# Kernel tuning notes

Measured on AMD Instinct MI355X. Metric: run time of the kernel, lower is better.

The kernel has to match this reference:

```python
import jax, jax.numpy as jnp
import numpy as np

N = 100000   # nodes
E = 1600000  # directed edges (avg degree 16)
IN, HID, OUT = 32, 64, 32


def setup_inputs() -> dict:
    key = jax.random.key(0)
    k0, k1, k2, k3 = jax.random.split(key, 4)
    x = jax.random.normal(k0, (N, IN), dtype=jnp.float32)
    edge_index = jax.random.randint(k1, (2, E), 0, N, dtype=jnp.int32)
    W1 = jax.random.normal(k2, (IN, HID), dtype=jnp.float32) * (1.0 / np.sqrt(IN))
    b1 = jnp.zeros((HID,), dtype=jnp.float32)
    W2 = jax.random.normal(k3, (HID, OUT), dtype=jnp.float32) * (1.0 / np.sqrt(HID))
    b2 = jnp.zeros((OUT,), dtype=jnp.float32)
    return {"x": x, "edge_index": edge_index, "W1": W1, "b1": b1, "W2": W2, "b2": b2}


def gcn_conv(x, src, dst, W, b, n):
    # GCNConv: D^{-1/2} (A + I) D^{-1/2} X W + b, deg computed after self-loops
    h = x @ W                                   # [N, d_out]
    ones = jnp.ones_like(dst, dtype=h.dtype)
    deg = jax.ops.segment_sum(ones, dst, num_segments=n)   # >= 1 (self-loops)
    dinv = jax.lax.rsqrt(jnp.maximum(deg, 1.0))
    norm = dinv[src] * dinv[dst]                # [E + N]
    agg = jax.ops.segment_sum(norm[:, None] * h[src], dst, num_segments=n)
    return agg + b


def reference(x, edge_index, W1, b1, W2, b2):
    n = x.shape[0]
    loop = jnp.arange(n, dtype=edge_index.dtype)
    src = jnp.concatenate([edge_index[0], loop])  # add self-loops once
    dst = jnp.concatenate([edge_index[1], loop])
    h = jax.nn.relu(gcn_conv(x, src, dst, W1, b1, n))
    # dropout omitted (eval mode)
    out = gcn_conv(h, src, dst, W2, b2, n)
    return out
```

## Files before the change

kernel.cpp:

```cpp
#include <hip/hip_runtime.h>

#define IN_F  32
#define HID_F 64
#define OUT_F 32

#define BKT_SHIFT 8
#define BKT_NODES 256
#define NBLK      128

__device__ inline unsigned short f2bf(float f) {
    unsigned u = __float_as_uint(f);
    return (unsigned short)((u + 0x7FFF + ((u >> 16) & 1)) >> 16);
}
__device__ inline float bf2f(unsigned short h) {
    return __uint_as_float(((unsigned)h) << 16);
}

__global__ __launch_bounds__(256) void count_kernel(const int* __restrict__ dst,
                                                    int* __restrict__ cnt, int E, int nb)
{
    __shared__ int hist[1024];
    int tid = threadIdx.x;
    for (int i = tid; i < nb; i += 256) hist[i] = 0;
    __syncthreads();
    for (int e = blockIdx.x * 256 + tid; e < E; e += NBLK * 256)
        atomicAdd(&hist[dst[e] >> BKT_SHIFT], 1);
    __syncthreads();
    for (int i = tid; i < nb; i += 256) cnt[i * NBLK + blockIdx.x] = hist[i];
}

__global__ __launch_bounds__(NBLK) void bsum_kernel(const int* __restrict__ cnt,
                                                    int* __restrict__ bsum)
{
    __shared__ int s[NBLK];
    int tid = threadIdx.x, b = blockIdx.x;
    s[tid] = cnt[b * NBLK + tid];
    __syncthreads();
    for (int off = NBLK / 2; off > 0; off >>= 1) {
        if (tid < off) s[tid] += s[tid + off];
        __syncthreads();
    }
    if (tid == 0) bsum[b] = s[0];
}

__global__ __launch_bounds__(512) void bscan_kernel(int* __restrict__ bsum, int nb,
                                                    int* __restrict__ cellstart, int nc,
                                                    int* __restrict__ rowstart, int n, int E)
{
    __shared__ int s[512];
    int tid = threadIdx.x;
    int my = (tid < nb) ? bsum[tid] : 0;
    s[tid] = my;
    __syncthreads();
    for (int off = 1; off < 512; off <<= 1) {
        int t = (tid >= off) ? s[tid - off] : 0;
        __syncthreads();
        s[tid] += t;
        __syncthreads();
    }
    if (tid < nb) bsum[tid] = s[tid] - my;
    if (tid == 0) { cellstart[nc] = E; rowstart[n] = E; }
}

__global__ __launch_bounds__(NBLK) void cscan_kernel(const int* __restrict__ cnt,
                                                     const int* __restrict__ bsum,
                                                     int* __restrict__ cellstart)
{
    __shared__ int s[NBLK];
    int tid = threadIdx.x, b = blockIdx.x;
    int my = cnt[b * NBLK + tid];
    s[tid] = my;
    __syncthreads();
    for (int off = 1; off < NBLK; off <<= 1) {
        int t = (tid >= off) ? s[tid - off] : 0;
        __syncthreads();
        s[tid] += t;
        __syncthreads();
    }
    cellstart[b * NBLK + tid] = bsum[b] + s[tid] - my;
}

__global__ __launch_bounds__(256) void append_kernel(
    const int* __restrict__ src, const int* __restrict__ dst,
    const int* __restrict__ cellstart, unsigned* __restrict__ pairs, int E, int nb)
{
    __shared__ int cur[1024];
    int tid = threadIdx.x;
    for (int i = tid; i < nb; i += 256) cur[i] = cellstart[i * NBLK + blockIdx.x];
    __syncthreads();
    for (int e = blockIdx.x * 256 + tid; e < E; e += NBLK * 256) {
        int d = dst[e];
        int pos = atomicAdd(&cur[d >> BKT_SHIFT], 1);
        pairs[pos] = ((unsigned)src[e] << BKT_SHIFT) | (unsigned)(d & (BKT_NODES - 1));
    }
}

__global__ __launch_bounds__(256) void place_kernel(
    const int* __restrict__ cellstart, const unsigned* __restrict__ pairs,
    int* __restrict__ srcs, int* __restrict__ rowstart, float* __restrict__ dinv, int n)
{
    __shared__ int hist[BKT_NODES];
    __shared__ int ofs[BKT_NODES];
    int b = blockIdx.x, tid = threadIdx.x;
    int beg = cellstart[b * NBLK], end = cellstart[(b + 1) * NBLK];
    hist[tid] = 0;
    __syncthreads();
    for (int e = beg + tid; e < end; e += 256)
        atomicAdd(&hist[pairs[e] & (BKT_NODES - 1)], 1);
    __syncthreads();
    int my = hist[tid];
    ofs[tid] = my;
    __syncthreads();
    for (int off = 1; off < 256; off <<= 1) {
        int t = (tid >= off) ? ofs[tid - off] : 0;
        __syncthreads();
        ofs[tid] += t;
        __syncthreads();
    }
    int excl = ofs[tid] - my;
    int node = b * BKT_NODES + tid;
    if (node < n) {
        rowstart[node] = beg + excl;
        dinv[node] = rsqrtf((float)(my + 1));
    }
    __syncthreads();
    ofs[tid] = excl;
    __syncthreads();
    for (int e = beg + tid; e < end; e += 256) {
        unsigned p = pairs[e];
        int dl = p & (BKT_NODES - 1);
        int pos = beg + atomicAdd(&ofs[dl], 1);
        srcs[pos] = (int)(p >> BKT_SHIFT);
    }
}

__global__ void xs_kernel(const float* __restrict__ x, const float* __restrict__ dinv,
                          unsigned short* __restrict__ xsb, int n) {
    int t = blockIdx.x * blockDim.x + threadIdx.x;
    if (t < n * (IN_F / 4)) {
        float d = dinv[t >> 3];
        float4 v = ((const float4*)x)[t];
        ushort4 o;
        o.x = f2bf(v.x * d); o.y = f2bf(v.y * d);
        o.z = f2bf(v.z * d); o.w = f2bf(v.w * d);
        ((ushort4*)xsb)[t] = o;
    }
}

__global__ __launch_bounds__(256) void fused1_kernel(
    const int* __restrict__ rowstart, const int* __restrict__ srcs,
    const unsigned short* __restrict__ xsb, const float* __restrict__ dinv,
    const float* __restrict__ b1, const float* __restrict__ W1,
    const float* __restrict__ W2, unsigned short* __restrict__ hs2b, int n)
{
    __shared__ float W1s[IN_F * HID_F];
    __shared__ float W2s[HID_F * OUT_F];
    __shared__ float grow[8][IN_F];
    __shared__ float hrow[8][HID_F];
    int tid = threadIdx.x;
    for (int t = tid; t < IN_F * HID_F; t += 256) W1s[t] = W1[t];
    for (int t = tid; t < HID_F * OUT_F; t += 256) W2s[t] = W2[t];

    int sub = tid >> 5;
    unsigned j = tid & 31;
    int node = blockIdx.x * 8 + sub;
    bool active = node < n;
    int nodec = active ? node : 0;

    int beg = rowstart[nodec], end = active ? rowstart[nodec + 1] : beg;
    float a0 = active ? bf2f(xsb[((unsigned)nodec << 5) + j]) : 0.f;
    float a1 = 0.f, a2 = 0.f, a3 = 0.f, a4 = 0.f, a5 = 0.f, a6 = 0.f, a7 = 0.f;
    int e = beg;
    for (; e + 8 <= end; e += 8) {
        unsigned o0 = ((unsigned)srcs[e]     << 5) + j, o1 = ((unsigned)srcs[e + 1] << 5) + j;
        unsigned o2 = ((unsigned)srcs[e + 2] << 5) + j, o3 = ((unsigned)srcs[e + 3] << 5) + j;
        unsigned o4 = ((unsigned)srcs[e + 4] << 5) + j, o5 = ((unsigned)srcs[e + 5] << 5) + j;
        unsigned o6 = ((unsigned)srcs[e + 6] << 5) + j, o7 = ((unsigned)srcs[e + 7] << 5) + j;
        a0 += bf2f(xsb[o0]); a1 += bf2f(xsb[o1]);
        a2 += bf2f(xsb[o2]); a3 += bf2f(xsb[o3]);
        a4 += bf2f(xsb[o4]); a5 += bf2f(xsb[o5]);
        a6 += bf2f(xsb[o6]); a7 += bf2f(xsb[o7]);
    }
    for (; e + 4 <= end; e += 4) {
        unsigned o0 = ((unsigned)srcs[e]     << 5) + j, o1 = ((unsigned)srcs[e + 1] << 5) + j;
        unsigned o2 = ((unsigned)srcs[e + 2] << 5) + j, o3 = ((unsigned)srcs[e + 3] << 5) + j;
        a0 += bf2f(xsb[o0]); a1 += bf2f(xsb[o1]);
        a2 += bf2f(xsb[o2]); a3 += bf2f(xsb[o3]);
    }
    for (; e < end; ++e) a0 += bf2f(xsb[((unsigned)srcs[e] << 5) + j]);
    float dv = dinv[nodec];
    grow[sub][j] = dv * (((a0 + a1) + (a2 + a3)) + ((a4 + a5) + (a6 + a7)));
    __syncthreads();

    float h0 = b1[j], h1v = b1[j + 32];
    #pragma unroll
    for (int k = 0; k < IN_F; ++k) {
        float gk = grow[sub][k];
        h0  += gk * W1s[k * HID_F + j];
        h1v += gk * W1s[k * HID_F + j + 32];
    }
    hrow[sub][j]      = fmaxf(h0, 0.f);
    hrow[sub][j + 32] = fmaxf(h1v, 0.f);
    __syncthreads();

    float p = 0.f;
    #pragma unroll
    for (int k = 0; k < HID_F; ++k) p += hrow[sub][k] * W2s[k * OUT_F + j];
    if (active) hs2b[((unsigned)node << 5) + j] = f2bf(dv * p);
}

__global__ __launch_bounds__(256) void agg2_kernel(
    const int* __restrict__ rowstart, const int* __restrict__ srcs,
    const unsigned short* __restrict__ hs2b, const float* __restrict__ dinv,
    const float* __restrict__ b2, float* __restrict__ out, int n)
{
    int t = blockIdx.x * blockDim.x + threadIdx.x;
    int node = t >> 5;
    if (node >= n) return;
    unsigned j = t & 31;
    int beg = rowstart[node], end = rowstart[node + 1];
    float a0 = bf2f(hs2b[((unsigned)node << 5) + j]);
    float a1 = 0.f, a2 = 0.f, a3 = 0.f, a4 = 0.f, a5 = 0.f, a6 = 0.f, a7 = 0.f;
    int e = beg;
    for (; e + 8 <= end; e += 8) {
        unsigned o0 = ((unsigned)srcs[e]     << 5) + j, o1 = ((unsigned)srcs[e + 1] << 5) + j;
        unsigned o2 = ((unsigned)srcs[e + 2] << 5) + j, o3 = ((unsigned)srcs[e + 3] << 5) + j;
        unsigned o4 = ((unsigned)srcs[e + 4] << 5) + j, o5 = ((unsigned)srcs[e + 5] << 5) + j;
        unsigned o6 = ((unsigned)srcs[e + 6] << 5) + j, o7 = ((unsigned)srcs[e + 7] << 5) + j;
        a0 += bf2f(hs2b[o0]); a1 += bf2f(hs2b[o1]);
        a2 += bf2f(hs2b[o2]); a3 += bf2f(hs2b[o3]);
        a4 += bf2f(hs2b[o4]); a5 += bf2f(hs2b[o5]);
        a6 += bf2f(hs2b[o6]); a7 += bf2f(hs2b[o7]);
    }
    for (; e + 4 <= end; e += 4) {
        unsigned o0 = ((unsigned)srcs[e]     << 5) + j, o1 = ((unsigned)srcs[e + 1] << 5) + j;
        unsigned o2 = ((unsigned)srcs[e + 2] << 5) + j, o3 = ((unsigned)srcs[e + 3] << 5) + j;
        a0 += bf2f(hs2b[o0]); a1 += bf2f(hs2b[o1]);
        a2 += bf2f(hs2b[o2]); a3 += bf2f(hs2b[o3]);
    }
    for (; e < end; ++e) a0 += bf2f(hs2b[((unsigned)srcs[e] << 5) + j]);
    out[(size_t)node * OUT_F + j] =
        dinv[node] * (((a0 + a1) + (a2 + a3)) + ((a4 + a5) + (a6 + a7))) + b2[j];
}

extern "C" void kernel_launch(void* const* d_in, const int* in_sizes, int n_in,
                              void* d_out, int out_size, void* d_ws, size_t ws_size,
                              hipStream_t stream) {
    const float* x  = (const float*)d_in[0];
    const int*   ei = (const int*)  d_in[1];
    const float* W1 = (const float*)d_in[2];
    const float* b1 = (const float*)d_in[3];
    const float* W2 = (const float*)d_in[4];
    const float* b2 = (const float*)d_in[5];
    float* out = (float*)d_out;

    const int n = in_sizes[0] / IN_F;
    const int E = in_sizes[1] / 2;
    const int* src = ei;
    const int* dst = ei + E;

    const int nb = (n + BKT_NODES - 1) >> BKT_SHIFT;
    const int nc = nb * NBLK;

    int* ip = (int*)d_ws;
    int* cnt       = ip;                 ip += nc;
    int* cellstart = ip;                 ip += nc + 1;
    int* bsum      = ip;                 ip += nb + 1;
    int* rowstart  = ip;                 ip += n + 1;
    unsigned* pairs = (unsigned*)ip;     ip += E;
    int* srcs_srt  = ip;                 ip += E;
    float* dinv = (float*)ip;            ip += n;
    unsigned short* xsb  = (unsigned short*)ip;
    ip += (size_t)n * IN_F / 2;
    unsigned short* hs2b = (unsigned short*)ip;

    count_kernel<<<NBLK, 256, 0, stream>>>(dst, cnt, E, nb);
    bsum_kernel <<<nb, NBLK, 0, stream>>>(cnt, bsum);
    bscan_kernel<<<1, 512, 0, stream>>>(bsum, nb, cellstart, nc, rowstart, n, E);
    cscan_kernel<<<nb, NBLK, 0, stream>>>(cnt, bsum, cellstart);
    append_kernel<<<NBLK, 256, 0, stream>>>(src, dst, cellstart, pairs, E, nb);
    place_kernel<<<nb, 256, 0, stream>>>(cellstart, pairs, srcs_srt, rowstart, dinv, n);

    xs_kernel<<<((size_t)n * 8 + 255) / 256, 256, 0, stream>>>(x, dinv, xsb, n);

    fused1_kernel<<<(n + 7) / 8, 256, 0, stream>>>(rowstart, srcs_srt, xsb, dinv, b1, W1, W2, hs2b, n);
    agg2_kernel<<<((size_t)n * 32 + 255) / 256, 256, 0, stream>>>(rowstart, srcs_srt, hs2b, dinv, b2, out, n);
}
```

Before: 256.4 us.

## Gather two bf16 features per lane with 16 lanes per node in aggregations

Both aggregation kernels now assign 16 threads per node and load packed 32-bit words holding two bf16 features, instead of 32 threads loading single 16-bit values. fused1 processes 16 nodes per block and its dense stages are remapped accordingly, with packed bf16 writes. The intent is to halve the per-edge load instruction count and make each row gather a 64-byte access with wider transactions. The cost is more accumulator registers per thread and more FMA work per thread in the dense stages.

```diff
diff --git a/kernel.cpp b/kernel.cpp
--- a/kernel.cpp
+++ b/kernel.cpp
@@ -12,9 +12,8 @@
     unsigned u = __float_as_uint(f);
     return (unsigned short)((u + 0x7FFF + ((u >> 16) & 1)) >> 16);
 }
-__device__ inline float bf2f(unsigned short h) {
-    return __uint_as_float(((unsigned)h) << 16);
-}
+__device__ inline float bflo(unsigned w) { return __uint_as_float(w << 16); }
+__device__ inline float bfhi(unsigned w) { return __uint_as_float(w & 0xFFFF0000u); }
 
 __global__ __launch_bounds__(256) void count_kernel(const int* __restrict__ dst,
                                                     int* __restrict__ cnt, int E, int nb)
@@ -149,98 +148,131 @@
 
 __global__ __launch_bounds__(256) void fused1_kernel(
     const int* __restrict__ rowstart, const int* __restrict__ srcs,
-    const unsigned short* __restrict__ xsb, const float* __restrict__ dinv,
+    const unsigned* __restrict__ xs2, const float* __restrict__ dinv,
     const float* __restrict__ b1, const float* __restrict__ W1,
-    const float* __restrict__ W2, unsigned short* __restrict__ hs2b, int n)
+    const float* __restrict__ W2, unsigned* __restrict__ hs2p, int n)
 {
     __shared__ float W1s[IN_F * HID_F];
     __shared__ float W2s[HID_F * OUT_F];
-    __shared__ float grow[8][IN_F];
-    __shared__ float hrow[8][HID_F];
+    __shared__ float grow[16][IN_F];
+    __shared__ float hrow[16][HID_F];
     int tid = threadIdx.x;
     for (int t = tid; t < IN_F * HID_F; t += 256) W1s[t] = W1[t];
     for (int t = tid; t < HID_F * OUT_F; t += 256) W2s[t] = W2[t];
 
-    int sub = tid >> 5;
-    unsigned j = tid & 31;
-    int node = blockIdx.x * 8 + sub;
+    int nl = tid >> 4;
+    unsigned q = tid & 15;
+    int node = blockIdx.x * 16 + nl;
     bool active = node < n;
     int nodec = active ? node : 0;
 
     int beg = rowstart[nodec], end = active ? rowstart[nodec + 1] : beg;
-    float a0 = active ? bf2f(xsb[((unsigned)nodec << 5) + j]) : 0.f;
-    float a1 = 0.f, a2 = 0.f, a3 = 0.f, a4 = 0.f, a5 = 0.f, a6 = 0.f, a7 = 0.f;
+    unsigned ws = active ? xs2[((unsigned)nodec << 4) + q] : 0u;
+    float a0l = bflo(ws), a0h = bfhi(ws);
+    float a1l = 0.f, a1h = 0.f, a2l = 0.f, a2h = 0.f, a3l = 0.f, a3h = 0.f;
+    float a4l = 0.f, a4h = 0.f, a5l = 0.f, a5h = 0.f, a6l = 0.f, a6h = 0.f;
+    float a7l = 0.f, a7h = 0.f;
     int e = beg;
     for (; e + 8 <= end; e += 8) {
-        unsigned o0 = ((unsigned)srcs[e]     << 5) + j, o1 = ((unsigned)srcs[e + 1] << 5) + j;
-        unsigned o2 = ((unsigned)srcs[e + 2] << 5) + j, o3 = ((unsigned)srcs[e + 3] << 5) + j;
-        unsigned o4 = ((unsigned)srcs[e + 4] << 5) + j, o5 = ((unsigned)srcs[e + 5] << 5) + j;
-        unsigned o6 = ((unsigned)srcs[e + 6] << 5) + j, o7 = ((unsigned)srcs[e + 7] << 5) + j;
-        a0 += bf2f(xsb[o0]); a1 += bf2f(xsb[o1]);
-        a2 += bf2f(xsb[o2]); a3 += bf2f(xsb[o3]);
-        a4 += bf2f(xsb[o4]); a5 += bf2f(xsb[o5]);
-        a6 += bf2f(xsb[o6]); a7 += bf2f(xsb[o7]);
+        unsigned o0 = ((unsigned)srcs[e]     << 4) + q, o1 = ((unsigned)srcs[e + 1] << 4) + q;
+        unsigned o2 = ((unsigned)srcs[e + 2] << 4) + q, o3 = ((unsigned)srcs[e + 3] << 4) + q;
+        unsigned o4 = ((unsigned)srcs[e + 4] << 4) + q, o5 = ((unsigned)srcs[e + 5] << 4) + q;
+        unsigned o6 = ((unsigned)srcs[e + 6] << 4) + q, o7 = ((unsigned)srcs[e + 7] << 4) + q;
+        unsigned w0 = xs2[o0], w1 = xs2[o1], w2 = xs2[o2], w3 = xs2[o3];
+        unsigned w4 = xs2[o4], w5 = xs2[o5], w6 = xs2[o6], w7 = xs2[o7];
+        a0l += bflo(w0); a0h += bfhi(w0); a1l += bflo(w1); a1h += bfhi(w1);
+        a2l += bflo(w2); a2h += bfhi(w2); a3l += bflo(w3); a3h += bfhi(w3);
+        a4l += bflo(w4); a4h += bfhi(w4); a5l += bflo(w5); a5h += bfhi(w5);
+        a6l += bflo(w6); a6h += bfhi(w6); a7l += bflo(w7); a7h += bfhi(w7);
     }
     for (; e + 4 <= end; e += 4) {
-        unsigned o0 = ((unsigned)srcs[e]     << 5) + j, o1 = ((unsigned)srcs[e + 1] << 5) + j;
-        unsigned o2 = ((unsigned)srcs[e + 2] << 5) + j, o3 = ((unsigned)srcs[e + 3] << 5) + j;
-        a0 += bf2f(xsb[o0]); a1 += bf2f(xsb[o1]);
-        a2 += bf2f(xsb[o2]); a3 += bf2f(xsb[o3]);
-    }
-    for (; e < end; ++e) a0 += bf2f(xsb[((unsigned)srcs[e] << 5) + j]);
+        unsigned o0 = ((unsigned)srcs[e]     << 4) + q, o1 = ((unsigned)srcs[e + 1] << 4) + q;
+        unsigned o2 = ((unsigned)srcs[e + 2] << 4) + q, o3 = ((unsigned)srcs[e + 3] << 4) + q;
+        unsigned w0 = xs2[o0], w1 = xs2[o1], w2 = xs2[o2], w3 = xs2[o3];
+        a0l += bflo(w0); a0h += bfhi(w0); a1l += bflo(w1); a1h += bfhi(w1);
+        a2l += bflo(w2); a2h += bfhi(w2); a3l += bflo(w3); a3h += bfhi(w3);
+    }
+    for (; e < end; ++e) {
+        unsigned w0 = xs2[((unsigned)srcs[e] << 4) + q];
+        a0l += bflo(w0); a0h += bfhi(w0);
+    }
     float dv = dinv[nodec];
-    grow[sub][j] = dv * (((a0 + a1) + (a2 + a3)) + ((a4 + a5) + (a6 + a7)));
-    __syncthreads();
-
-    float h0 = b1[j], h1v = b1[j + 32];
+    grow[nl][2 * q]     = dv * (((a0l + a1l) + (a2l + a3l)) + ((a4l + a5l) + (a6l + a7l)));
+    grow[nl][2 * q + 1] = dv * (((a0h + a1h) + (a2h + a3h)) + ((a4h + a5h) + (a6h + a7h)));
+    __syncthreads();
+
+    float h0 = b1[q], h1 = b1[q + 16], h2 = b1[q + 32], h3 = b1[q + 48];
     #pragma unroll
     for (int k = 0; k < IN_F; ++k) {
-        float gk = grow[sub][k];
-        h0  += gk * W1s[k * HID_F + j];
-        h1v += gk * W1s[k * HID_F + j + 32];
-    }
-    hrow[sub][j]      = fmaxf(h0, 0.f);
-    hrow[sub][j + 32] = fmaxf(h1v, 0.f);
-    __syncthreads();
-
-    float p = 0.f;
+        float gk = grow[nl][k];
+        h0 += gk * W1s[k * HID_F + q];
+        h1 += gk * W1s[k * HID_F + q + 16];
+        h2 += gk * W1s[k * HID_F + q + 32];
+        h3 += gk * W1s[k * HID_F + q + 48];
+    }
+    hrow[nl][q]      = fmaxf(h0, 0.f);
+    hrow[nl][q + 16] = fmaxf(h1, 0.f);
+    hrow[nl][q + 32] = fmaxf(h2, 0.f);
+    hrow[nl][q + 48] = fmaxf(h3, 0.f);
+    __syncthreads();
+
+    float p0 = 0.f, p1 = 0.f;
     #pragma unroll
-    for (int k = 0; k < HID_F; ++k) p += hrow[sub][k] * W2s[k * OUT_F + j];
-    if (active) hs2b[((unsigned)node << 5) + j] = f2bf(dv * p);
+    for (int k = 0; k < HID_F; ++k) {
+        float hk = hrow[nl][k];
+        p0 += hk * W2s[k * OUT_F + 2 * q];
+        p1 += hk * W2s[k * OUT_F + 2 * q + 1];
+    }
+    if (active) {
+        unsigned pack = (unsigned)f2bf(dv * p0) | ((unsigned)f2bf(dv * p1) << 16);
+        hs2p[((unsigned)node << 4) + q] = pack;
+    }
 }
 
 __global__ __launch_bounds__(256) void agg2_kernel(
     const int* __restrict__ rowstart, const int* __restrict__ srcs,
-    const unsigned short* __restrict__ hs2b, const float* __restrict__ dinv,
+    const unsigned* __restrict__ hs2p, const float* __restrict__ dinv,
     const float* __restrict__ b2, float* __restrict__ out, int n)
 {
     int t = blockIdx.x * blockDim.x + threadIdx.x;
-    int node = t >> 5;
+    int node = t >> 4;
     if (node >= n) return;
-    unsigned j = t & 31;
+    unsigned q = t & 15;
     int beg = rowstart[node], end = rowstart[node + 1];
-    float a0 = bf2f(hs2b[((unsigned)node << 5) + j]);
-    float a1 = 0.f, a2 = 0.f, a3 = 0.f, a4 = 0.f, a5 = 0.f, a6 = 0.f, a7 = 0.f;
+    unsigned ws = hs2p[((unsigned)node << 4) + q];
+    float a0l = bflo(ws), a0h = bfhi(ws);
+    float a1l = 0.f, a1h = 0.f, a2l = 0.f, a2h = 0.f, a3l = 0.f, a3h = 0.f;
+    float a4l = 0.f, a4h = 0.f, a5l = 0.f, a5h = 0.f, a6l = 0.f, a6h = 0.f;
+    float a7l = 0.f, a7h = 0.f;
     int e = beg;
     for (; e + 8 <= end; e += 8) {
-        unsigned o0 = ((unsigned)srcs[e]     << 5) + j, o1 = ((unsigned)srcs[e + 1] << 5) + j;
-        unsigned o2 = ((unsigned)srcs[e + 2] << 5) + j, o3 = ((unsigned)srcs[e + 3] << 5) + j;
-        unsigned o4 = ((unsigned)srcs[e + 4] << 5) + j, o5 = ((unsigned)srcs[e + 5] << 5) + j;
-        unsigned o6 = ((unsigned)srcs[e + 6] << 5) + j, o7 = ((unsigned)srcs[e + 7] << 5) + j;
-        a0 += bf2f(hs2b[o0]); a1 += bf2f(hs2b[o1]);
-        a2 += bf2f(hs2b[o2]); a3 += bf2f(hs2b[o3]);
-        a4 += bf2f(hs2b[o4]); a5 += bf2f(hs2b[o5]);
-        a6 += bf2f(hs2b[o6]); a7 += bf2f(hs2b[o7]);
+        unsigned o0 = ((unsigned)srcs[e]     << 4) + q, o1 = ((unsigned)srcs[e + 1] << 4) + q;
+        unsigned o2 = ((unsigned)srcs[e + 2] << 4) + q, o3 = ((unsigned)srcs[e + 3] << 4) + q;
+        unsigned o4 = ((unsigned)srcs[e + 4] << 4) + q, o5 = ((unsigned)srcs[e + 5] << 4) + q;
+        unsigned o6 = ((unsigned)srcs[e + 6] << 4) + q, o7 = ((unsigned)srcs[e + 7] << 4) + q;
+        unsigned w0 = hs2p[o0], w1 = hs2p[o1], w2 = hs2p[o2], w3 = hs2p[o3];
+        unsigned w4 = hs2p[o4], w5 = hs2p[o5], w6 = hs2p[o6], w7 = hs2p[o7];
+        a0l += bflo(w0); a0h += bfhi(w0); a1l += bflo(w1); a1h += bfhi(w1);
+        a2l += bflo(w2); a2h += bfhi(w2); a3l += bflo(w3); a3h += bfhi(w3);
+        a4l += bflo(w4); a4h += bfhi(w4); a5l += bflo(w5); a5h += bfhi(w5);
+        a6l += bflo(w6); a6h += bfhi(w6); a7l += bflo(w7); a7h += bfhi(w7);
     }
     for (; e + 4 <= end; e += 4) {
-        unsigned o0 = ((unsigned)srcs[e]     << 5) + j, o1 = ((unsigned)srcs[e + 1] << 5) + j;
-        unsigned o2 = ((unsigned)srcs[e + 2] << 5) + j, o3 = ((unsigned)srcs[e + 3] << 5) + j;
-        a0 += bf2f(hs2b[o0]); a1 += bf2f(hs2b[o1]);
-        a2 += bf2f(hs2b[o2]); a3 += bf2f(hs2b[o3]);
-    }
-    for (; e < end; ++e) a0 += bf2f(hs2b[((unsigned)srcs[e] << 5) + j]);
-    out[(size_t)node * OUT_F + j] =
-        dinv[node] * (((a0 + a1) + (a2 + a3)) + ((a4 + a5) + (a6 + a7))) + b2[j];
+        unsigned o0 = ((unsigned)srcs[e]     << 4) + q, o1 = ((unsigned)srcs[e + 1] << 4) + q;
+        unsigned o2 = ((unsigned)srcs[e + 2] << 4) + q, o3 = ((unsigned)srcs[e + 3] << 4) + q;
+        unsigned w0 = hs2p[o0], w1 = hs2p[o1], w2 = hs2p[o2], w3 = hs2p[o3];
+        a0l += bflo(w0); a0h += bfhi(w0); a1l += bflo(w1); a1h += bfhi(w1);
+        a2l += bflo(w2); a2h += bfhi(w2); a3l += bflo(w3); a3h += bfhi(w3);
+    }
+    for (; e < end; ++e) {
+        unsigned w0 = hs2p[((unsigned)srcs[e] << 4) + q];
+        a0l += bflo(w0); a0h += bfhi(w0);
+    }
+    float dvv = dinv[node];
+    float2 r;
+    r.x = dvv * (((a0l + a1l) + (a2l + a3l)) + ((a4l + a5l) + (a6l + a7l))) + b2[2 * q];
+    r.y = dvv * (((a0h + a1h) + (a2h + a3h)) + ((a4h + a5h) + (a6h + a7h))) + b2[2 * q + 1];
+    ((float2*)out)[((size_t)node << 4) + q] = r;
 }
 
 extern "C" void kernel_launch(void* const* d_in, const int* in_sizes, int n_in,
@@ -270,9 +302,8 @@
     unsigned* pairs = (unsigned*)ip;     ip += E;
     int* srcs_srt  = ip;                 ip += E;
     float* dinv = (float*)ip;            ip += n;
-    unsigned short* xsb  = (unsigned short*)ip;
-    ip += (size_t)n * IN_F / 2;
-    unsigned short* hs2b = (unsigned short*)ip;
+    unsigned* xs2  = (unsigned*)ip;      ip += (size_t)n * IN_F / 2;
+    unsigned* hs2p = (unsigned*)ip;
 
     count_kernel<<<NBLK, 256, 0, stream>>>(dst, cnt, E, nb);
     bsum_kernel <<<nb, NBLK, 0, stream>>>(cnt, bsum);
@@ -281,8 +312,8 @@
     append_kernel<<<NBLK, 256, 0, stream>>>(src, dst, cellstart, pairs, E, nb);
     place_kernel<<<nb, 256, 0, stream>>>(cellstart, pairs, srcs_srt, rowstart, dinv, n);
 
-    xs_kernel<<<((size_t)n * 8 + 255) / 256, 256, 0, stream>>>(x, dinv, xsb, n);
-
-    fused1_kernel<<<(n + 7) / 8, 256, 0, stream>>>(rowstart, srcs_srt, xsb, dinv, b1, W1, W2, hs2b, n);
-    agg2_kernel<<<((size_t)n * 32 + 255) / 256, 256, 0, stream>>>(rowstart, srcs_srt, hs2b, dinv, b2, out, n);
-}
+    xs_kernel<<<((size_t)n * 8 + 255) / 256, 256, 0, stream>>>(x, dinv, (unsigned short*)xs2, n);
+
+    fused1_kernel<<<(n + 15) / 16, 256, 0, stream>>>(rowstart, srcs_srt, xs2, dinv, b1, W1, W2, hs2p, n);
+    agg2_kernel<<<((size_t)n * 16 + 255) / 256, 256, 0, stream>>>(rowstart, srcs_srt, hs2p, dinv, b2, out, n);
+}
```

After: 235.2 us. -8.3%, faster.
